# Optimization experiments

Measured on AMD Instinct MI355X. Metric: run time of the kernel, lower is better.

Reference implementation:

```python
import jax, jax.numpy as jnp
import numpy as np

D_IN = 1024
D_OUT = 1024
SEQ = 4096


def setup_inputs() -> dict:
    key = jax.random.key(0)
    kx, kq, kk, kv = jax.random.split(key, 4)
    x = jax.random.normal(kx, (SEQ, D_IN), dtype=jnp.float32)
    # torch Linear weights: [d_out, d_in], y = x @ W.T; no bias (qkv_bias=False)
    s = 1.0 / np.sqrt(D_IN)
    Wq = jax.random.uniform(kq, (D_OUT, D_IN), dtype=jnp.float32, minval=-s, maxval=s)
    Wk = jax.random.uniform(kk, (D_OUT, D_IN), dtype=jnp.float32, minval=-s, maxval=s)
    Wv = jax.random.uniform(kv, (D_OUT, D_IN), dtype=jnp.float32, minval=-s, maxval=s)
    return {"x": x, "Wq": Wq, "Wk": Wk, "Wv": Wv}


def reference(x, Wq, Wk, Wv):
    seq = x.shape[0]
    q = x @ Wq.T  # [S, d_out]
    k = x @ Wk.T
    v = x @ Wv.T
    scores = q @ k.T  # [S, S]
    # causal mask: positions j > i masked to -inf (triu, diagonal=1)
    causal = jnp.tril(jnp.ones((seq, seq), dtype=bool))
    scores = jnp.where(causal, scores, -jnp.inf)
    attn = jax.nn.softmax(scores / jnp.sqrt(jnp.float32(q.shape[-1])), axis=-1)
    return attn @ v  # [S, d_out]
```

## Files before the change

### kernel.cpp

```cpp
#include <hip/hip_runtime.h>
#include <hip/hip_bf16.h>
#include <cstdint>
#include <cstddef>


#define SEQQ 4096
#define DDIM 1024

typedef __bf16 bf16x8 __attribute__((ext_vector_type(8)));
typedef float f32x4 __attribute__((ext_vector_type(4)));

__device__ __forceinline__ unsigned short f2bf(float f) {
  unsigned int u = __builtin_bit_cast(unsigned int, f);
  unsigned int r = u + 0x7FFFu + ((u >> 16) & 1u);
  return (unsigned short)(r >> 16);
}

__device__ __forceinline__ void gload_lds16(const void* g, void* lds) {
  __builtin_amdgcn_global_load_lds(
      (__attribute__((address_space(1))) void*)(uintptr_t)g,
      (__attribute__((address_space(3))) void*)(uintptr_t)lds, 16, 0, 0);
}

__global__ __launch_bounds__(256) void cvt_all(const float* __restrict__ x,
                                               const float* __restrict__ Wq,
                                               const float* __restrict__ Wk,
                                               const float* __restrict__ Wv,
                                               unsigned short* __restrict__ xb,
                                               unsigned short* __restrict__ Wcat) {
  int b = blockIdx.x;
  const float* src;
  unsigned short* dst;
  float scale = 1.0f;
  if (b < 4096) {
    src = x; dst = xb;
  } else if (b < 5120) {
    src = Wq; dst = Wcat; scale = 0.03125f; b -= 4096;
  } else if (b < 6144) {
    src = Wk; dst = Wcat + (1u << 20); b -= 5120;
  } else {
    src = Wv; dst = Wcat + (2u << 20); b -= 6144;
  }
  const int i = (b * 256 + threadIdx.x) * 4;
  const float4 v = *reinterpret_cast<const float4*>(src + i);
  ushort4 o;
  o.x = f2bf(v.x * scale);
  o.y = f2bf(v.y * scale);
  o.z = f2bf(v.z * scale);
  o.w = f2bf(v.w * scale);
  *reinterpret_cast<ushort4*>(dst + i) = o;
}

#define GEMM_PRE()                                                          \
  __shared__ unsigned short As[3][8192] __attribute__((aligned(16)));       \
  __shared__ unsigned short Bs[3][8192] __attribute__((aligned(16)));       \
  const int tid = threadIdx.x;                                              \
  const int wave = tid >> 6, lane = tid & 63;                               \
  const int wr = (wave >> 2) * 128, wc = (wave & 3) * 64;                   \
  f32x4 acc[8][4] = {};                                                     \
  int offA[8], offB[4];                                                     \
  {                                                                         \
    const int cb = (lane >> 4) * 16;                                        \
    const int rA = wr + (lane & 15);                                        \
    _Pragma("unroll")                                                       \
    for (int m = 0; m < 8; ++m) {                                           \
      int o = (rA + m * 16) * 64 + cb;                                      \
      offA[m] = o ^ (((o >> 9) & 1) << 5);                                  \
    }                                                                       \
    const int rB = wc + (lane & 15);                                        \
    _Pragma("unroll")                                                       \
    for (int n = 0; n < 4; ++n) {                                           \
      int o = (rB + n * 16) * 64 + cb;                                      \
      offB[n] = o ^ (((o >> 9) & 1) << 5);                                  \
    }                                                                       \
  }

#define GEMM_LOOP(ABASE, LDA, BBASE, LDB, S0, S1)                           \
  do {                                                                      \
    const int nt = (S1) - (S0);                                             \
    const char *pA0, *pA1, *pB0, *pB1;                                      \
    {                                                                       \
      const size_t srow = wave * 16 + (lane >> 2);                          \
      const int scb = ((lane & 3) * 16) ^ (((lane >> 5) & 1) << 5);         \
      pA0 = (const char*)(ABASE) + srow * ((size_t)(LDA) * 2) +             \
            (size_t)(S0) * 64 + scb;                                        \
      pA1 = pA0 + (size_t)128 * ((size_t)(LDA) * 2);                        \
      pB0 = (const char*)(BBASE) + srow * ((size_t)(LDB) * 2) +             \
            (size_t)(S0) * 64 + scb;                                        \
      pB1 = pB0 + (size_t)128 * ((size_t)(LDB) * 2);                        \
    }                                                                       \
    char* ldsA = (char*)&As[0][0];                                          \
    char* ldsB = (char*)&Bs[0][0];                                          \
    const int wofs = wave * 1024;                                           \
    gload_lds16(pA0, ldsA + wofs);                                          \
    gload_lds16(pA1, ldsA + 8192 + wofs);                                   \
    gload_lds16(pB0, ldsB + wofs);                                          \
    gload_lds16(pB1, ldsB + 8192 + wofs);                                   \
    pA0 += 64; pA1 += 64; pB0 += 64; pB1 += 64;                             \
    if (nt > 1) {                                                           \
      gload_lds16(pA0, ldsA + 16384 + wofs);                                \
      gload_lds16(pA1, ldsA + 16384 + 8192 + wofs);                         \
      gload_lds16(pB0, ldsB + 16384 + wofs);                                \
      gload_lds16(pB1, ldsB + 16384 + 8192 + wofs);                         \
      pA0 += 64; pA1 += 64; pB0 += 64; pB1 += 64;                           \
      asm volatile("s_waitcnt vmcnt(4)" ::: "memory");                      \
    } else {                                                                \
      asm volatile("s_waitcnt vmcnt(0)" ::: "memory");                      \
    }                                                                       \
    asm volatile("s_barrier" ::: "memory");                                 \
    int rb = 0;                                                             \
    for (int s = 0; s < nt; ++s) {                                          \
      const int bofs = rb * 16384;                                          \
      bf16x8 a[8], b[4];                                                    \
      _Pragma("unroll")                                                     \
      for (int m = 0; m < 8; ++m)                                           \
        a[m] = *(const bf16x8*)(ldsA + bofs + offA[m]);                     \
      _Pragma("unroll")                                                     \
      for (int n = 0; n < 4; ++n)                                           \
        b[n] = *(const bf16x8*)(ldsB + bofs + offB[n]);                     \
      if (s + 2 < nt) {                                                     \
        const int wofs2 = ((rb >= 1) ? rb - 1 : 2) * 16384 + wofs;          \
        gload_lds16(pA0, ldsA + wofs2);                                     \
        gload_lds16(pA1, ldsA + wofs2 + 8192);                              \
        gload_lds16(pB0, ldsB + wofs2);                                     \
        gload_lds16(pB1, ldsB + wofs2 + 8192);                              \
        pA0 += 64; pA1 += 64; pB0 += 64; pB1 += 64;                         \
        asm volatile("s_waitcnt lgkmcnt(0)" ::: "memory");                  \
        asm volatile("s_waitcnt vmcnt(4)" ::: "memory");                    \
      } else if (s + 1 < nt) {                                              \
        asm volatile("s_waitcnt lgkmcnt(0)" ::: "memory");                  \
        asm volatile("s_waitcnt vmcnt(0)" ::: "memory");                    \
      } else {                                                              \
        asm volatile("s_waitcnt lgkmcnt(0)" ::: "memory");                  \
      }                                                                     \
      asm volatile("s_barrier" ::: "memory");                               \
      __builtin_amdgcn_s_setprio(1);                                        \
      _Pragma("unroll")                                                     \
      for (int m = 0; m < 8; ++m)                                           \
        _Pragma("unroll")                                                   \
        for (int n = 0; n < 4; ++n)                                         \
          acc[m][n] = __builtin_amdgcn_mfma_f32_16x16x32_bf16(              \
              a[m], b[n], acc[m][n], 0, 0, 0);                              \
      __builtin_amdgcn_s_setprio(0);                                        \
      rb = (rb == 2) ? 0 : rb + 1;                                          \
    }                                                                       \
  } while (0)

__device__ __forceinline__ int xcd_swz(int id, int n) {
  return (id & 7) * (n >> 3) + (id >> 3);
}

__global__ __launch_bounds__(512, 1) void gemm_qkv(const unsigned short* __restrict__ X,
                                                   const unsigned short* __restrict__ W,
                                                   unsigned short* __restrict__ Qb,
                                                   unsigned short* __restrict__ Kb,
                                                   unsigned short* __restrict__ Vt) {
  const int id = xcd_swz(blockIdx.x, 192);
  const int by = id / 12, bx = id - by * 12;
  GEMM_PRE();
  const int brow = by * 256, bcol = bx * 256;
  GEMM_LOOP(X + (size_t)brow * DDIM, DDIM, W + (size_t)bcol * DDIM, DDIM, 0, 32);
  const int region = bcol >> 10;
  const int lcol = bcol & 1023;
  const int c0 = wc + (lane & 15);
  const int r0 = wr + ((lane >> 4) << 2);
  if (region < 2) {
    unsigned short* dst = (region == 0) ? Qb : Kb;
#pragma unroll
    for (int m = 0; m < 8; ++m) {
      const int r = brow + r0 + m * 16;
#pragma unroll
      for (int n = 0; n < 4; ++n) {
        const int c = lcol + c0 + n * 16;
#pragma unroll
        for (int j = 0; j < 4; ++j)
          dst[(size_t)(r + j) * DDIM + c] = f2bf(acc[m][n][j]);
      }
    }
  } else {
#pragma unroll
    for (int m = 0; m < 8; ++m) {
      const int r = brow + r0 + m * 16;
#pragma unroll
      for (int n = 0; n < 4; ++n) {
        const int c = lcol + c0 + n * 16;
        ushort4 pk;
        pk.x = f2bf(acc[m][n][0]);
        pk.y = f2bf(acc[m][n][1]);
        pk.z = f2bf(acc[m][n][2]);
        pk.w = f2bf(acc[m][n][3]);
        *reinterpret_cast<ushort4*>(Vt + (size_t)c * SEQQ + r) = pk;
      }
    }
  }
}

__global__ __launch_bounds__(512, 1) void gemm_qkt(const unsigned short* __restrict__ Qb,
                                                   const unsigned short* __restrict__ Kb,
                                                   unsigned short* __restrict__ S) {
  const int id = xcd_swz(blockIdx.x, 136);
  int bi = (int)((sqrtf(8.0f * (float)id + 1.0f) - 1.0f) * 0.5f);
  while ((bi + 1) * (bi + 2) / 2 <= id) ++bi;
  while (bi * (bi + 1) / 2 > id) --bi;
  const int bj = id - bi * (bi + 1) / 2;
  GEMM_PRE();
  const int brow = bi * 256, bcol = bj * 256;
  GEMM_LOOP(Qb + (size_t)brow * DDIM, DDIM, Kb + (size_t)bcol * DDIM, DDIM, 0, 32);
  const int c0 = wc + (lane & 15);
  const int r0 = wr + ((lane >> 4) << 2);
#pragma unroll
  for (int m = 0; m < 8; ++m) {
    const int r = brow + r0 + m * 16;
#pragma unroll
    for (int n = 0; n < 4; ++n) {
      const int c = bcol + c0 + n * 16;
#pragma unroll
      for (int j = 0; j < 4; ++j) {
        unsigned short o = (c > r + j) ? (unsigned short)0
                                       : f2bf(__expf(acc[m][n][j]));
        S[(size_t)(r + j) * SEQQ + c] = o;
      }
    }
  }
}

__global__ __launch_bounds__(256) void rowinv_kernel(const unsigned short* __restrict__ S,
                                                     float* __restrict__ rowinv) {
  const int row = blockIdx.x;
  const int L = ((row >> 8) + 1) << 8;
  const unsigned short* Srow = S + (size_t)row * SEQQ;
  __shared__ float red[4];
  const int tid = threadIdx.x, lane = tid & 63, wave = tid >> 6;
  float sum = 0.f;
  for (int j = tid * 8; j < L; j += 2048) {
    const uint4 v = *reinterpret_cast<const uint4*>(Srow + j);
    const unsigned u[4] = {v.x, v.y, v.z, v.w};
#pragma unroll
    for (int q = 0; q < 4; ++q) {
      sum += __builtin_bit_cast(float, u[q] << 16);
      sum += __builtin_bit_cast(float, u[q] & 0xFFFF0000u);
    }
  }
#pragma unroll
  for (int o = 32; o; o >>= 1) sum += __shfl_xor(sum, o);
  if (lane == 0) red[wave] = sum;
  __syncthreads();
  if (tid == 0) rowinv[row] = 1.0f / (red[0] + red[1] + red[2] + red[3]);
}

__device__ __forceinline__ int pv_nc(int bi) { return (bi >> 2) + 1; }
__device__ __forceinline__ int pv_rcbase(int bi) {
  const int g = bi >> 2, r = bi & 3;
  return 2 * g * (g - 1) + r * g;
}

__global__ __launch_bounds__(512, 1) void gemm_pv_split(const unsigned short* __restrict__ P,
                                                        const unsigned short* __restrict__ Vt,
                                                        const float* __restrict__ rowinv,
                                                        float* __restrict__ O,
                                                        float* __restrict__ part) {
  const int id = xcd_swz(blockIdx.x, 256);
  const int bj = id & 3, bi = (id >> 2) & 15, ck = id >> 6;
  const int nc = pv_nc(bi);
  if (ck >= nc) return;
  const int kt = (bi + 1) * 8;
  const int W = (kt + nc - 1) / nc;
  const int s0 = ck * W;
  const int s1 = min(s0 + W, kt);
  if (s0 >= s1) return;

  GEMM_PRE();
  const int brow = bi * 256, bcol = bj * 256;
  GEMM_LOOP(P + (size_t)brow * SEQQ, SEQQ, Vt + (size_t)bcol * SEQQ, SEQQ, s0, s1);
  const int c0 = wc + (lane & 15);
  const int r0 = wr + ((lane >> 4) << 2);
  if (ck == 0) {
#pragma unroll
    for (int m = 0; m < 8; ++m) {
      const int r = brow + r0 + m * 16;
#pragma unroll
      for (int j = 0; j < 4; ++j) {
        const float ri = rowinv[r + j];
#pragma unroll
        for (int n = 0; n < 4; ++n) {
          const int c = bcol + c0 + n * 16;
          O[(size_t)(r + j) * DDIM + c] = acc[m][n][j] * ri;
        }
      }
    }
  } else {
    float* tile = part + ((size_t)(pv_rcbase(bi) + (ck - 1)) * 4 + bj) * 65536;
#pragma unroll
    for (int m = 0; m < 8; ++m) {
      const int lr = r0 + m * 16;
#pragma unroll
      for (int j = 0; j < 4; ++j) {
        const float ri = rowinv[brow + lr + j];
#pragma unroll
        for (int n = 0; n < 4; ++n) {
          const int lc = c0 + n * 16;
          tile[(lr + j) * 256 + lc] = acc[m][n][j] * ri;
        }
      }
    }
  }
}

__global__ __launch_bounds__(256) void reduce_pv(float* __restrict__ O,
                                                 const float* __restrict__ part) {
  const int idx = blockIdx.x * 256 + threadIdx.x;
  const int r = 1024 + (idx >> 8);
  const int cc = (idx & 255) * 4;
  const int bi = r >> 8;
  const int nparts = bi >> 2;
  const int rcb = pv_rcbase(bi);
  const int bj = cc >> 8;
  const int lr = r & 255, lc = cc & 255;
  float4 acc = *reinterpret_cast<float4*>(O + (size_t)r * DDIM + cc);
  for (int k = 0; k < nparts; ++k) {
    const float4 p = *reinterpret_cast<const float4*>(
        part + ((size_t)(rcb + k) * 4 + bj) * 65536 + lr * 256 + lc);
    acc.x += p.x; acc.y += p.y; acc.z += p.z; acc.w += p.w;
  }
  *reinterpret_cast<float4*>(O + (size_t)r * DDIM + cc) = acc;
}

extern "C" void kernel_launch(void* const* d_in, const int* in_sizes, int n_in,
                              void* d_out, int out_size, void* d_ws, size_t ws_size,
                              hipStream_t stream) {
  (void)in_sizes; (void)n_in; (void)out_size; (void)ws_size;
  const float* x = (const float*)d_in[0];
  const float* Wq = (const float*)d_in[1];
  const float* Wk = (const float*)d_in[2];
  const float* Wv = (const float*)d_in[3];
  float* out = (float*)d_out;

  char* ws = (char*)d_ws;
  unsigned short* xb   = (unsigned short*)(ws);
  unsigned short* Wcat = (unsigned short*)(ws + ((size_t)8 << 20));
  unsigned short* Qb   = (unsigned short*)(ws + ((size_t)14 << 20));
  unsigned short* Kb   = (unsigned short*)(ws + ((size_t)22 << 20));
  unsigned short* Vt   = (unsigned short*)(ws + ((size_t)30 << 20));
  unsigned short* S    = (unsigned short*)(ws + ((size_t)38 << 20));
  float* part   = (float*)ws;
  float* rowinv = (float*)(ws + ((size_t)24 << 20));

  cvt_all<<<7168, 256, 0, stream>>>(x, Wq, Wk, Wv, xb, Wcat);
  gemm_qkv<<<192, 512, 0, stream>>>(xb, Wcat, Qb, Kb, Vt);
  gemm_qkt<<<136, 512, 0, stream>>>(Qb, Kb, S);
  rowinv_kernel<<<SEQQ, 256, 0, stream>>>(S, rowinv);
  gemm_pv_split<<<256, 512, 0, stream>>>(S, Vt, rowinv, out, part);
  reduce_pv<<<3072, 256, 0, stream>>>(out, part);
}
```

Measured before the change: 124.7 us.

## Fuse softmax row sums into QK^T epilogue and store PV partials in bf16

The QK^T epilogue now accumulates exp values per row, reduces them across lanes with shuffles, and writes per-tile, per-wave partial sums. A small combine kernel turns these into reciprocal row sums, so the separate pass that re-read the whole bf16 score matrix is gone. Split-K PV partials are now written as bf16 into a separate buffer for every chunk, and the reduce kernel sums them instead of adding into O. This cuts memory traffic but adds bf16 rounding to the partial outputs and an extra small launch.

```diff
diff --git a/kernel.cpp b/kernel.cpp
--- a/kernel.cpp
+++ b/kernel.cpp
@@ -14,6 +14,10 @@
   unsigned int u = __builtin_bit_cast(unsigned int, f);
   unsigned int r = u + 0x7FFFu + ((u >> 16) & 1u);
   return (unsigned short)(r >> 16);
+}
+
+__device__ __forceinline__ float bf2f(unsigned short b) {
+  return __builtin_bit_cast(float, (unsigned int)b << 16);
 }
 
 __device__ __forceinline__ void gload_lds16(const void* g, void* lds) {
@@ -197,7 +201,8 @@
 
 __global__ __launch_bounds__(512, 1) void gemm_qkt(const unsigned short* __restrict__ Qb,
                                                    const unsigned short* __restrict__ Kb,
-                                                   unsigned short* __restrict__ S) {
+                                                   unsigned short* __restrict__ S,
+                                                   float* __restrict__ tsw) {
   const int id = xcd_swz(blockIdx.x, 136);
   int bi = (int)((sqrtf(8.0f * (float)id + 1.0f) - 1.0f) * 0.5f);
   while ((bi + 1) * (bi + 2) / 2 <= id) ++bi;
@@ -208,57 +213,58 @@
   GEMM_LOOP(Qb + (size_t)brow * DDIM, DDIM, Kb + (size_t)bcol * DDIM, DDIM, 0, 32);
   const int c0 = wc + (lane & 15);
   const int r0 = wr + ((lane >> 4) << 2);
+  float* tswp = tsw + ((size_t)id * 4 + (wave & 3)) * 256;
 #pragma unroll
   for (int m = 0; m < 8; ++m) {
     const int r = brow + r0 + m * 16;
+    float rs[4] = {0.f, 0.f, 0.f, 0.f};
 #pragma unroll
     for (int n = 0; n < 4; ++n) {
       const int c = bcol + c0 + n * 16;
 #pragma unroll
       for (int j = 0; j < 4; ++j) {
-        unsigned short o = (c > r + j) ? (unsigned short)0
-                                       : f2bf(__expf(acc[m][n][j]));
-        S[(size_t)(r + j) * SEQQ + c] = o;
-      }
-    }
-  }
-}
-
-__global__ __launch_bounds__(256) void rowinv_kernel(const unsigned short* __restrict__ S,
-                                                     float* __restrict__ rowinv) {
-  const int row = blockIdx.x;
-  const int L = ((row >> 8) + 1) << 8;
-  const unsigned short* Srow = S + (size_t)row * SEQQ;
-  __shared__ float red[4];
-  const int tid = threadIdx.x, lane = tid & 63, wave = tid >> 6;
-  float sum = 0.f;
-  for (int j = tid * 8; j < L; j += 2048) {
-    const uint4 v = *reinterpret_cast<const uint4*>(Srow + j);
-    const unsigned u[4] = {v.x, v.y, v.z, v.w};
-#pragma unroll
-    for (int q = 0; q < 4; ++q) {
-      sum += __builtin_bit_cast(float, u[q] << 16);
-      sum += __builtin_bit_cast(float, u[q] & 0xFFFF0000u);
-    }
-  }
-#pragma unroll
-  for (int o = 32; o; o >>= 1) sum += __shfl_xor(sum, o);
-  if (lane == 0) red[wave] = sum;
-  __syncthreads();
-  if (tid == 0) rowinv[row] = 1.0f / (red[0] + red[1] + red[2] + red[3]);
+        const float e = (c > r + j) ? 0.0f : __expf(acc[m][n][j]);
+        rs[j] += e;
+        S[(size_t)(r + j) * SEQQ + c] = (c > r + j) ? (unsigned short)0
+                                                    : f2bf(e);
+      }
+    }
+#pragma unroll
+    for (int j = 0; j < 4; ++j) {
+#pragma unroll
+      for (int o = 8; o; o >>= 1) rs[j] += __shfl_xor(rs[j], o);
+    }
+    if ((lane & 15) == 0) {
+#pragma unroll
+      for (int j = 0; j < 4; ++j) tswp[r0 + m * 16 + j] = rs[j];
+    }
+  }
+}
+
+__global__ __launch_bounds__(256) void combine_rowinv(const float* __restrict__ tsw,
+                                                      float* __restrict__ rowinv) {
+  const int r = blockIdx.x * 256 + threadIdx.x;
+  const int bi = r >> 8, lr = r & 255;
+  const int t0 = bi * (bi + 1) / 2;
+  float s = 0.f;
+  for (int t = t0; t <= t0 + bi; ++t) {
+#pragma unroll
+    for (int w = 0; w < 4; ++w) s += tsw[((size_t)t * 4 + w) * 256 + lr];
+  }
+  rowinv[r] = 1.0f / s;
 }
 
 __device__ __forceinline__ int pv_nc(int bi) { return (bi >> 2) + 1; }
-__device__ __forceinline__ int pv_rcbase(int bi) {
-  const int g = bi >> 2, r = bi & 3;
-  return 2 * g * (g - 1) + r * g;
+__device__ __forceinline__ int pv_rcbase2(int bi) {
+  const int g = bi >> 2;
+  return (g == 1) ? (bi - 4) * 2 : (g == 2) ? 8 + (bi - 8) * 3 : 20 + (bi - 12) * 4;
 }
 
 __global__ __launch_bounds__(512, 1) void gemm_pv_split(const unsigned short* __restrict__ P,
                                                         const unsigned short* __restrict__ Vt,
                                                         const float* __restrict__ rowinv,
                                                         float* __restrict__ O,
-                                                        float* __restrict__ part) {
+                                                        unsigned short* __restrict__ partB) {
   const int id = xcd_swz(blockIdx.x, 256);
   const int bj = id & 3, bi = (id >> 2) & 15, ck = id >> 6;
   const int nc = pv_nc(bi);
@@ -274,7 +280,7 @@
   GEMM_LOOP(P + (size_t)brow * SEQQ, SEQQ, Vt + (size_t)bcol * SEQQ, SEQQ, s0, s1);
   const int c0 = wc + (lane & 15);
   const int r0 = wr + ((lane >> 4) << 2);
-  if (ck == 0) {
+  if (bi < 4) {
 #pragma unroll
     for (int m = 0; m < 8; ++m) {
       const int r = brow + r0 + m * 16;
@@ -289,7 +295,8 @@
       }
     }
   } else {
-    float* tile = part + ((size_t)(pv_rcbase(bi) + (ck - 1)) * 4 + bj) * 65536;
+    unsigned short* tile =
+        partB + ((size_t)(pv_rcbase2(bi) + ck) * 4 + bj) * 65536;
 #pragma unroll
     for (int m = 0; m < 8; ++m) {
       const int lr = r0 + m * 16;
@@ -299,7 +306,7 @@
 #pragma unroll
         for (int n = 0; n < 4; ++n) {
           const int lc = c0 + n * 16;
-          tile[(lr + j) * 256 + lc] = acc[m][n][j] * ri;
+          tile[(lr + j) * 256 + lc] = f2bf(acc[m][n][j] * ri);
         }
       }
     }
@@ -307,22 +314,22 @@
 }
 
 __global__ __launch_bounds__(256) void reduce_pv(float* __restrict__ O,
-                                                 const float* __restrict__ part) {
+                                                 const unsigned short* __restrict__ partB) {
   const int idx = blockIdx.x * 256 + threadIdx.x;
   const int r = 1024 + (idx >> 8);
   const int cc = (idx & 255) * 4;
   const int bi = r >> 8;
-  const int nparts = bi >> 2;
-  const int rcb = pv_rcbase(bi);
+  const int nc = pv_nc(bi);
+  const int rcb = pv_rcbase2(bi);
   const int bj = cc >> 8;
   const int lr = r & 255, lc = cc & 255;
-  float4 acc = *reinterpret_cast<float4*>(O + (size_t)r * DDIM + cc);
-  for (int k = 0; k < nparts; ++k) {
-    const float4 p = *reinterpret_cast<const float4*>(
-        part + ((size_t)(rcb + k) * 4 + bj) * 65536 + lr * 256 + lc);
-    acc.x += p.x; acc.y += p.y; acc.z += p.z; acc.w += p.w;
-  }
-  *reinterpret_cast<float4*>(O + (size_t)r * DDIM + cc) = acc;
+  float4 a = make_float4(0.f, 0.f, 0.f, 0.f);
+  for (int k = 0; k < nc; ++k) {
+    const ushort4 p = *reinterpret_cast<const ushort4*>(
+        partB + ((size_t)(rcb + k) * 4 + bj) * 65536 + lr * 256 + lc);
+    a.x += bf2f(p.x); a.y += bf2f(p.y); a.z += bf2f(p.z); a.w += bf2f(p.w);
+  }
+  *reinterpret_cast<float4*>(O + (size_t)r * DDIM + cc) = a;
 }
 
 extern "C" void kernel_launch(void* const* d_in, const int* in_sizes, int n_in,
@@ -342,13 +349,14 @@
   unsigned short* Kb   = (unsigned short*)(ws + ((size_t)22 << 20));
   unsigned short* Vt   = (unsigned short*)(ws + ((size_t)30 << 20));
   unsigned short* S    = (unsigned short*)(ws + ((size_t)38 << 20));
-  float* part   = (float*)ws;
-  float* rowinv = (float*)(ws + ((size_t)24 << 20));
+  float* tsw            = (float*)ws;
+  float* rowinv         = (float*)(ws + ((size_t)1 << 20));
+  unsigned short* partB = (unsigned short*)(ws + ((size_t)2 << 20));
 
   cvt_all<<<7168, 256, 0, stream>>>(x, Wq, Wk, Wv, xb, Wcat);
   gemm_qkv<<<192, 512, 0, stream>>>(xb, Wcat, Qb, Kb, Vt);
-  gemm_qkt<<<136, 512, 0, stream>>>(Qb, Kb, S);
-  rowinv_kernel<<<SEQQ, 256, 0, stream>>>(S, rowinv);
-  gemm_pv_split<<<256, 512, 0, stream>>>(S, Vt, rowinv, out, part);
-  reduce_pv<<<3072, 256, 0, stream>>>(out, part);
-}
+  gemm_qkt<<<136, 512, 0, stream>>>(Qb, Kb, S, tsw);
+  combine_rowinv<<<16, 256, 0, stream>>>(tsw, rowinv);
+  gemm_pv_split<<<256, 512, 0, stream>>>(S, Vt, rowinv, out, partB);
+  reduce_pv<<<3072, 256, 0, stream>>>(out, partB);
+}
```

Result: no change. 124.5 us (-0.2%).
